# Optimization experiments

Measured on AMD Instinct MI355X. Metric: run time of the kernel, lower is better.

Reference implementation:

```python
import jax, jax.numpy as jnp
import numpy as np

N, D, K, V, H, F_ = 4096, 128, 64, 64, 4, 256
EPS = 1e-5


def _layer_norm(x, g, b):
    m = jnp.mean(x, axis=-1, keepdims=True)
    v = jnp.mean((x - m) ** 2, axis=-1, keepdims=True)
    return (x - m) * jax.lax.rsqrt(v + EPS) * g + b


def setup_inputs() -> dict:
    key = jax.random.key(0)
    ks = jax.random.split(key, 20)
    s_in = (2.0 / D) ** 0.5  # kaiming-ish scale for q/k/v projections
    inp = {
        "x": jax.random.normal(ks[0], (N, D), jnp.float32),
        "rpe": jax.random.normal(ks[1], (5, N, N), jnp.float32) * 0.02,
        "Wq": jax.random.normal(ks[2], (H, D, K), jnp.float32) * s_in,
        "bq": jnp.zeros((H, K), jnp.float32),
        "Wk": jax.random.normal(ks[3], (H, D, K), jnp.float32) * s_in,
        "bk": jnp.zeros((H, K), jnp.float32),
        "Wv": jax.random.normal(ks[4], (H, D, V), jnp.float32) * s_in,
        "bv": jnp.zeros((H, V), jnp.float32),
        "rpe_w": jax.random.normal(ks[5], (5,), jnp.float32) * (1.0 / 5.0) ** 0.5,
        "rpe_b": jnp.zeros((), jnp.float32),
        "Wo": jax.random.normal(ks[6], (H * V, D), jnp.float32) * (1.0 / (H * V)) ** 0.5,
        "bo": jnp.zeros((D,), jnp.float32),
        "W1": jax.random.normal(ks[7], (D, F_), jnp.float32) * (1.0 / D) ** 0.5,
        "b1": jnp.zeros((F_,), jnp.float32),
        "W2": jax.random.normal(ks[8], (F_, D), jnp.float32) * (1.0 / F_) ** 0.5,
        "b2": jnp.zeros((D,), jnp.float32),
        "ln1_g": jnp.ones((D,), jnp.float32),
        "ln1_b": jnp.zeros((D,), jnp.float32),
        "ln2_g": jnp.ones((D,), jnp.float32),
        "ln2_b": jnp.zeros((D,), jnp.float32),
    }
    return inp


def reference(x, rpe, Wq, bq, Wk, bk, Wv, bv, rpe_w, rpe_b, Wo, bo,
              W1, b1, W2, b2, ln1_g, ln1_b, ln2_g, ln2_b):
    # ReLU'd per-head projections (vectorized over heads): [H, N, K/V]
    q = jax.nn.relu(jnp.einsum("nd,hdk->hnk", x, Wq) + bq[:, None, :])
    k = jax.nn.relu(jnp.einsum("nd,hdk->hnk", x, Wk) + bk[:, None, :])
    v = jax.nn.relu(jnp.einsum("nd,hdv->hnv", x, Wv) + bv[:, None, :])
    scores = jnp.einsum("hnk,hmk->hnm", q, k) / jnp.sqrt(jnp.asarray(K, x.dtype))
    attn = jax.nn.softmax(scores, axis=-1)  # torch dim=1 on 2D == last axis
    o = jnp.einsum("hnm,hmv->hnv", attn, v)
    mho = jnp.transpose(o, (1, 0, 2)).reshape(N, H * V)  # concat heads
    # RPE: Linear(5->1) over channel axis -> [N, N], then left-matmul
    rpe_weights = jnp.einsum("fnm,f->nm", rpe, rpe_w) + rpe_b
    adjusted = rpe_weights @ mho
    proj = adjusted @ Wo + bo
    x1 = _layer_norm(x + proj, ln1_g, ln1_b)  # dropout is identity (eval)
    ffn = jax.nn.relu(x1 @ W1 + b1) @ W2 + b2
    return _layer_norm(x1 + ffn, ln2_g, ln2_b)
```

## Files before the change

kernel.cpp:

```cpp
#include <hip/hip_runtime.h>

typedef __attribute__((ext_vector_type(8))) short bf16x8;
typedef __attribute__((ext_vector_type(4))) float f32x4;

#define N_TOK 4096
#define NC_ATT 8
#define NC_GEMM 8

static __device__ __forceinline__ ushort f2bf(float f) {
    union { float f; unsigned u; } x; x.f = f;
    unsigned u = x.u;
    unsigned r = (u + 0x7FFFu + ((u >> 16) & 1u)) >> 16;
    return (ushort)r;
}
static __device__ __forceinline__ unsigned pkbf(float a, float b) {
    unsigned r;
    asm("v_cvt_pk_bf16_f32 %0, %1, %2" : "=v"(r) : "v"(a), "v"(b));
    return r;
}
static __device__ __forceinline__ float bf2f(ushort u) {
    union { unsigned u; float f; } x; x.u = (unsigned)u << 16; return x.f;
}

__global__ void prep_all(const float* __restrict__ x,
                         const float* __restrict__ Wq, const float* __restrict__ Wk,
                         const float* __restrict__ Wv, const float* __restrict__ Wo,
                         const float* __restrict__ W1, const float* __restrict__ W2,
                         ushort* __restrict__ xb, ushort* __restrict__ WqT,
                         ushort* __restrict__ WkT, ushort* __restrict__ WvT,
                         ushort* __restrict__ WoT, ushort* __restrict__ W1T,
                         ushort* __restrict__ W2T) {
    int i = blockIdx.x * 256 + threadIdx.x;
    if (i < 131072) {
        float4 v = ((const float4*)x)[i];
        ushort4 o;
        o.x = f2bf(v.x); o.y = f2bf(v.y); o.z = f2bf(v.z); o.w = f2bf(v.w);
        ((ushort4*)xb)[i] = o;
        return;
    }
    int j = i - 131072;
    int t = j >> 15, e = j & 32767;
    if (t < 3) {
        const float* src = (t == 0 ? Wq : t == 1 ? Wk : Wv);
        ushort* dst = (t == 0 ? WqT : t == 1 ? WkT : WvT);
        int h = e >> 13, rem = e & 8191, d = rem >> 6, k = rem & 63;
        dst[h * 8192 + k * 128 + d] = f2bf(src[e]);
    } else if (t == 3) {
        int r = e >> 7, c = e & 127;
        WoT[c * 256 + r] = f2bf(Wo[e]);
    } else if (t == 4) {
        int r = e >> 8, c = e & 255;
        W1T[c * 128 + r] = f2bf(W1[e]);
    } else {
        int r = e >> 7, c = e & 127;
        W2T[c * 256 + r] = f2bf(W2[e]);
    }
}

__global__ __launch_bounds__(256) void qkv_proj(
    const ushort* __restrict__ xb, const ushort* __restrict__ WqT,
    const ushort* __restrict__ WkT, const ushort* __restrict__ WvT,
    const float* __restrict__ bq, const float* __restrict__ bk, const float* __restrict__ bv,
    ushort* __restrict__ qb, ushort* __restrict__ kb, ushort* __restrict__ vT) {
    int m0 = blockIdx.x * 64;
    int h = blockIdx.y & 3, which = blockIdx.y >> 2;
    int wave = threadIdx.x >> 6, lane = threadIdx.x & 63;
    int fr = lane & 15, kg = lane >> 4;
    int wm = m0 + wave * 16;
    const ushort* WT = (which == 0 ? WqT : which == 1 ? WkT : WvT) + (long)h * 64 * 128;
    const float* bias = (which == 0 ? bq : which == 1 ? bk : bv) + h * 64;
    f32x4 acc[4] = {};
    for (int k0 = 0; k0 < 128; k0 += 32) {
        bf16x8 a = *(const bf16x8*)(xb + (long)(wm + fr) * 128 + k0 + kg * 8);
#pragma unroll
        for (int t = 0; t < 4; ++t) {
            bf16x8 b = *(const bf16x8*)(WT + (long)(t * 16 + fr) * 128 + k0 + kg * 8);
            acc[t] = __builtin_amdgcn_mfma_f32_16x16x32_bf16(a, b, acc[t], 0, 0, 0);
        }
    }
    int rb = wm + kg * 4;
#pragma unroll
    for (int t = 0; t < 4; ++t) {
        int col = t * 16 + fr;
        float bs = bias[col];
        if (which == 2) {
            ushort4 o;
            o.x = f2bf(fmaxf(acc[t][0] + bs, 0.f));
            o.y = f2bf(fmaxf(acc[t][1] + bs, 0.f));
            o.z = f2bf(fmaxf(acc[t][2] + bs, 0.f));
            o.w = f2bf(fmaxf(acc[t][3] + bs, 0.f));
            *(ushort4*)(vT + ((long)h * 64 + col) * N_TOK + rb) = o;
        } else {
            ushort* dst = (which == 0 ? qb : kb) + (long)h * N_TOK * 64;
            float scl = (which == 0) ? 0.125f * 1.44269504f : 1.0f;
#pragma unroll
            for (int r = 0; r < 4; ++r)
                dst[(long)(rb + r) * 64 + col] = f2bf(fmaxf(acc[t][r] + bs, 0.f) * scl);
        }
    }
}

__global__ __launch_bounds__(512, 6) void fused_rpe_attn(
    const float* __restrict__ rpe, const float* __restrict__ rpe_w,
    const float* __restrict__ rpe_b, ushort* __restrict__ rpeW,
    const ushort* __restrict__ qb, const ushort* __restrict__ kb,
    const ushort* __restrict__ vT, ushort* __restrict__ opart,
    float* __restrict__ mlpart) {
    __shared__ ushort Kt[2][64 * 64];
    __shared__ ushort Vt[2][64 * 64];
    __shared__ ushort Pl[8][16 * 64];
    int bid = blockIdx.x;
    int idx = bid >> 1;
    if ((bid & 1) == 0) {
        const long QUADS = (long)N_TOK * N_TOK / 4;
        float w0 = rpe_w[0], w1 = rpe_w[1], w2 = rpe_w[2], w3 = rpe_w[3], w4 = rpe_w[4];
        float bb = rpe_b[0];
        const float4* p = (const float4*)rpe;
        for (long i = (long)idx * 512 + threadIdx.x; i < QUADS; i += (long)1024 * 512) {
            float4 a0 = p[i];
            float4 a1 = p[i + QUADS];
            float4 a2 = p[i + 2 * QUADS];
            float4 a3 = p[i + 3 * QUADS];
            float4 a4 = p[i + 4 * QUADS];
            ushort4 o;
            unsigned lo = pkbf(bb + w0 * a0.x + w1 * a1.x + w2 * a2.x + w3 * a3.x + w4 * a4.x,
                               bb + w0 * a0.y + w1 * a1.y + w2 * a2.y + w3 * a3.y + w4 * a4.y);
            unsigned hi = pkbf(bb + w0 * a0.z + w1 * a1.z + w2 * a2.z + w3 * a3.z + w4 * a4.z,
                               bb + w0 * a0.w + w1 * a1.w + w2 * a2.w + w3 * a3.w + w4 * a4.w);
            o.x = (ushort)lo; o.y = (ushort)(lo >> 16);
            o.z = (ushort)hi; o.w = (ushort)(hi >> 16);
            ((ushort4*)rpeW)[i] = o;
        }
        return;
    }
    int qt = idx & 31, h = (idx >> 5) & 3, cz = idx >> 7;
    int w = threadIdx.x >> 6, lane = threadIdx.x & 63;
    int fr = lane & 15, kg = lane >> 4;
    int lr = lane >> 3, lc = lane & 7;
    int swz = (lc ^ (lr & 7)) * 8;
    const ushort* qh = qb + (long)h * N_TOK * 64;
    const ushort* kh = kb + (long)h * N_TOK * 64;
    const ushort* vh = vT + (long)h * 64 * N_TOK;
    int q0 = qt * 128 + w * 16;
    bf16x8 qf0 = *(const bf16x8*)(qh + (long)(q0 + fr) * 64 + kg * 8);
    bf16x8 qf1 = *(const bf16x8*)(qh + (long)(q0 + fr) * 64 + 32 + kg * 8);
    f32x4 o[4] = {};
    float lsum = 0.f;
    int nbase = cz * (N_TOK / NC_ATT);
    auto stage = [&](int buf, int s) {
        int n0 = nbase + s * 64;
        int row = w * 8 + lr;
        __builtin_amdgcn_global_load_lds(
            (const __attribute__((address_space(1))) unsigned int*)(kh + (long)(n0 + row) * 64 + swz),
            (__attribute__((address_space(3))) unsigned int*)(&Kt[buf][w * 512]), 16, 0, 0);
        __builtin_amdgcn_global_load_lds(
            (const __attribute__((address_space(1))) unsigned int*)(vh + (long)row * N_TOK + n0 + swz),
            (__attribute__((address_space(3))) unsigned int*)(&Vt[buf][w * 512]), 16, 0, 0);
    };
    stage(0, 0);
    __syncthreads();
    const int NS = (N_TOK / NC_ATT) / 64;
    for (int s = 0; s < NS; ++s) {
        int buf = s & 1;
        if (s + 1 < NS) stage(buf ^ 1, s + 1);
        f32x4 sc[4] = {};
        __builtin_amdgcn_s_setprio(1);
#pragma unroll
        for (int t = 0; t < 4; ++t) {
            int row = t * 16 + fr;
            bf16x8 k0 = *(const bf16x8*)(&Kt[buf][row * 64 + ((kg * 8) ^ ((row & 7) * 8))]);
            bf16x8 k1 = *(const bf16x8*)(&Kt[buf][row * 64 + ((32 + kg * 8) ^ ((row & 7) * 8))]);
            sc[t] = __builtin_amdgcn_mfma_f32_16x16x32_bf16(k0, qf0, sc[t], 0, 0, 0);
            sc[t] = __builtin_amdgcn_mfma_f32_16x16x32_bf16(k1, qf1, sc[t], 0, 0, 0);
        }
        __builtin_amdgcn_s_setprio(0);
#pragma unroll
        for (int t = 0; t < 4; ++t)
#pragma unroll
            for (int r = 0; r < 4; ++r) {
                float p = exp2f(sc[t][r]);
                sc[t][r] = p;
                lsum += p;
            }
#pragma unroll
        for (int t = 0; t < 4; ++t) {
            uint2 u;
            u.x = pkbf(sc[t][0], sc[t][1]);
            u.y = pkbf(sc[t][2], sc[t][3]);
            *(uint2*)(&Pl[w][fr * 64 + ((t * 16 + kg * 4) ^ ((fr & 7) * 8))]) = u;
        }
        __builtin_amdgcn_s_setprio(1);
#pragma unroll
        for (int ks = 0; ks < 2; ++ks) {
            bf16x8 pf = *(const bf16x8*)(&Pl[w][fr * 64 + ((ks * 32 + kg * 8) ^ ((fr & 7) * 8))]);
#pragma unroll
            for (int t = 0; t < 4; ++t) {
                int row = t * 16 + fr;
                bf16x8 b = *(const bf16x8*)(&Vt[buf][row * 64 + ((ks * 32 + kg * 8) ^ ((row & 7) * 8))]);
                o[t] = __builtin_amdgcn_mfma_f32_16x16x32_bf16(pf, b, o[t], 0, 0, 0);
            }
        }
        __builtin_amdgcn_s_setprio(0);
        __syncthreads();
    }
    lsum += __shfl_xor(lsum, 16);
    lsum += __shfl_xor(lsum, 32);
    float linv = 1.0f / lsum;
    float lq[4];
#pragma unroll
    for (int r = 0; r < 4; ++r) lq[r] = __shfl(linv, kg * 4 + r);
    ushort* ob = opart + (((long)cz * 4 + h) * N_TOK + q0 + kg * 4) * 64;
#pragma unroll
    for (int t = 0; t < 4; ++t)
#pragma unroll
        for (int r = 0; r < 4; ++r)
            ob[(long)r * 64 + t * 16 + fr] = f2bf(o[t][r] * lq[r]);
    if (lane < 16)
        mlpart[((long)cz * 4 + h) * N_TOK + q0 + lane] = lsum;
}

__global__ __launch_bounds__(256) void combine_wo(
    const ushort* __restrict__ opart, const float* __restrict__ mlpart,
    const ushort* __restrict__ WoT, ushort* __restrict__ PT) {
    int q0 = blockIdx.x * 16;
    int tid = threadIdx.x;
    __shared__ ushort mt[16 * 256];
    {
        int q = tid >> 4, cg = tid & 15;
        int h = cg >> 2;
        long qg = q0 + q;
        float L = 0.f, co[NC_ATT];
#pragma unroll
        for (int c = 0; c < NC_ATT; ++c) {
            co[c] = mlpart[((long)c * 4 + h) * N_TOK + qg];
            L += co[c];
        }
        float inv = 1.0f / L;
#pragma unroll
        for (int c = 0; c < NC_ATT; ++c) co[c] *= inv;
        float a[16];
#pragma unroll
        for (int j = 0; j < 16; ++j) a[j] = 0.f;
#pragma unroll
        for (int c = 0; c < NC_ATT; ++c) {
            const ushort* pr = opart + (((long)c * 4 + h) * N_TOK + qg) * 64 + (cg & 3) * 16;
            bf16x8 v0 = *(const bf16x8*)(pr);
            bf16x8 v1 = *(const bf16x8*)(pr + 8);
#pragma unroll
            for (int j = 0; j < 8; ++j) {
                a[j] += co[c] * bf2f((ushort)v0[j]);
                a[8 + j] += co[c] * bf2f((ushort)v1[j]);
            }
        }
        int c0 = cg * 16;
#pragma unroll
        for (int g = 0; g < 4; ++g) {
            uint2 u;
            u.x = pkbf(a[g * 4 + 0], a[g * 4 + 1]);
            u.y = pkbf(a[g * 4 + 2], a[g * 4 + 3]);
            *(uint2*)(&mt[q * 256 + ((c0 + g * 4) ^ ((q & 7) * 8))]) = u;
        }
    }
    __syncthreads();
    {
        int w = tid >> 6, lane = tid & 63;
        int fr = lane & 15, kg = lane >> 4;
        f32x4 acc[2] = {};
        for (int k0 = 0; k0 < 256; k0 += 32) {
            bf16x8 a0 = *(const bf16x8*)(WoT + (long)(w * 32 + fr) * 256 + k0 + kg * 8);
            bf16x8 a1 = *(const bf16x8*)(WoT + (long)(w * 32 + 16 + fr) * 256 + k0 + kg * 8);
            bf16x8 b = *(const bf16x8*)(&mt[fr * 256 + ((k0 + kg * 8) ^ ((fr & 7) * 8))]);
            acc[0] = __builtin_amdgcn_mfma_f32_16x16x32_bf16(a0, b, acc[0], 0, 0, 0);
            acc[1] = __builtin_amdgcn_mfma_f32_16x16x32_bf16(a1, b, acc[1], 0, 0, 0);
        }
#pragma unroll
        for (int dt = 0; dt < 2; ++dt)
#pragma unroll
            for (int r = 0; r < 4; ++r)
                PT[(long)(w * 32 + dt * 16 + kg * 4 + r) * N_TOK + q0 + fr] =
                    f2bf(acc[dt][r]);
    }
}

__global__ __launch_bounds__(512) void gemm_big2(
    const ushort* __restrict__ A, const ushort* __restrict__ PT,
    float* __restrict__ part) {
    int mt = blockIdx.x, cz = blockIdx.y;
    int tid = threadIdx.x;
    int w = tid >> 6, lane = tid & 63;
    int fr = lane & 15, kg = lane >> 4;
    int lr = lane >> 3, lc = lane & 7;
    int swz = (lc ^ (lr & 7)) * 8;
    int ms = w >> 1, nh = w & 1;
    __shared__ ushort At[2][64 * 64];
    __shared__ ushort Bt[2][128 * 64];
    int m0 = mt * 64;
    long kbase = (long)cz * (N_TOK / NC_GEMM);
    int arow = ms * 16 + fr;
    auto stage = [&](int buf, int s) {
        long kc = kbase + s * 64 + swz;
        int rowA = w * 8 + lr;
        __builtin_amdgcn_global_load_lds(
            (const __attribute__((address_space(1))) unsigned int*)(A + (long)(m0 + rowA) * N_TOK + kc),
            (__attribute__((address_space(3))) unsigned int*)(&At[buf][w * 512]), 16, 0, 0);
#pragma unroll
        for (int j = 0; j < 2; ++j) {
            int row = w * 16 + j * 8 + lr;
            __builtin_amdgcn_global_load_lds(
                (const __attribute__((address_space(1))) unsigned int*)(PT + (long)row * N_TOK + kc),
                (__attribute__((address_space(3))) unsigned int*)(&Bt[buf][(w * 2 + j) * 512]), 16, 0, 0);
        }
    };
    f32x4 acc[4] = {};
    stage(0, 0);
    __syncthreads();
    const int NS = (N_TOK / NC_GEMM) / 64;
    for (int s = 0; s < NS; ++s) {
        int buf = s & 1;
        if (s + 1 < NS) stage(buf ^ 1, s + 1);
        __builtin_amdgcn_s_setprio(1);
#pragma unroll
        for (int ks = 0; ks < 2; ++ks) {
            int c = ks * 32 + kg * 8;
            bf16x8 av = *(const bf16x8*)(&At[buf][arow * 64 + (c ^ ((arow & 7) * 8))]);
#pragma unroll
            for (int nf = 0; nf < 4; ++nf) {
                int row = nh * 64 + nf * 16 + fr;
                bf16x8 b = *(const bf16x8*)(&Bt[buf][row * 64 + (c ^ ((row & 7) * 8))]);
                acc[nf] = __builtin_amdgcn_mfma_f32_16x16x32_bf16(av, b, acc[nf], 0, 0, 0);
            }
        }
        __builtin_amdgcn_s_setprio(0);
        __syncthreads();
    }
    float* pb = part + ((long)cz * N_TOK + m0 + ms * 16 + kg * 4) * 128 + nh * 64 + fr;
#pragma unroll
    for (int nf = 0; nf < 4; ++nf)
#pragma unroll
        for (int r = 0; r < 4; ++r)
            pb[(long)r * 128 + nf * 16] = acc[nf][r];
}

__global__ __launch_bounds__(256) void megatail(
    const float* __restrict__ gpart, const float* __restrict__ bo,
    const float* __restrict__ x, const float* __restrict__ g1,
    const float* __restrict__ lb1, const ushort* __restrict__ W1T,
    const float* __restrict__ b1, const ushort* __restrict__ W2T,
    const float* __restrict__ b2, const float* __restrict__ g2,
    const float* __restrict__ lb2, float* __restrict__ out) {
    int r0 = blockIdx.x * 16;
    int tid = threadIdx.x;
    int w = tid >> 6, lane = tid & 63;
    int fr = lane & 15, kg = lane >> 4;
    __shared__ float x1f[16][132];
    __shared__ ushort x1b[16][128];
    __shared__ ushort hbuf[16][256];
    __shared__ float otile[16][132];
    int row = tid >> 4, c0 = (tid & 15) * 8;
    {
        float v[8];
        float4 s0 = {0.f, 0.f, 0.f, 0.f}, s1 = {0.f, 0.f, 0.f, 0.f};
#pragma unroll
        for (int c = 0; c < NC_GEMM; ++c) {
            const float* pr = gpart + ((long)c * N_TOK + r0 + row) * 128 + c0;
            float4 a = *(const float4*)(pr);
            float4 b = *(const float4*)(pr + 4);
            s0.x += a.x; s0.y += a.y; s0.z += a.z; s0.w += a.w;
            s1.x += b.x; s1.y += b.y; s1.z += b.z; s1.w += b.w;
        }
        const float* xr = x + (long)(r0 + row) * 128 + c0;
        v[0] = s0.x + bo[c0 + 0] + xr[0];
        v[1] = s0.y + bo[c0 + 1] + xr[1];
        v[2] = s0.z + bo[c0 + 2] + xr[2];
        v[3] = s0.w + bo[c0 + 3] + xr[3];
        v[4] = s1.x + bo[c0 + 4] + xr[4];
        v[5] = s1.y + bo[c0 + 5] + xr[5];
        v[6] = s1.z + bo[c0 + 6] + xr[6];
        v[7] = s1.w + bo[c0 + 7] + xr[7];
        float s = 0.f;
#pragma unroll
        for (int jj = 0; jj < 8; ++jj) s += v[jj];
#pragma unroll
        for (int off = 1; off < 16; off <<= 1) s += __shfl_xor(s, off);
        float mean = s * (1.0f / 128.0f);
        float ss = 0.f;
#pragma unroll
        for (int jj = 0; jj < 8; ++jj) { float d = v[jj] - mean; ss += d * d; }
#pragma unroll
        for (int off = 1; off < 16; off <<= 1) ss += __shfl_xor(ss, off);
        float rstd = rsqrtf(ss * (1.0f / 128.0f) + 1e-5f);
        union { bf16x8 vec; ushort us[8]; } pk8;
#pragma unroll
        for (int jj = 0; jj < 8; ++jj) {
            float y = (v[jj] - mean) * rstd * g1[c0 + jj] + lb1[c0 + jj];
            x1f[row][c0 + jj] = y;
            pk8.us[jj] = f2bf(y);
        }
        *(bf16x8*)(&x1b[row][c0 ^ ((row & 7) * 8)]) = pk8.vec;
    }
    __syncthreads();
    {
        f32x4 a1[4] = {};
#pragma unroll
        for (int ks = 0; ks < 4; ++ks) {
            bf16x8 a = *(const bf16x8*)(&x1b[fr][(ks * 32 + kg * 8) ^ ((fr & 7) * 8)]);
#pragma unroll
            for (int t = 0; t < 4; ++t) {
                bf16x8 b = *(const bf16x8*)(W1T + (long)(w * 64 + t * 16 + fr) * 128 + ks * 32 + kg * 8);
                a1[t] = __builtin_amdgcn_mfma_f32_16x16x32_bf16(a, b, a1[t], 0, 0, 0);
            }
        }
#pragma unroll
        for (int t = 0; t < 4; ++t) {
            int col = w * 64 + t * 16 + fr;
            float bs = b1[col];
#pragma unroll
            for (int r = 0; r < 4; ++r) {
                int rr = kg * 4 + r;
                hbuf[rr][col ^ ((rr & 7) * 8)] = f2bf(fmaxf(a1[t][r] + bs, 0.f));
            }
        }
    }
    __syncthreads();
    {
        f32x4 a2[2] = {};
#pragma unroll
        for (int ks = 0; ks < 8; ++ks) {
            bf16x8 a = *(const bf16x8*)(&hbuf[fr][(ks * 32 + kg * 8) ^ ((fr & 7) * 8)]);
#pragma unroll
            for (int t = 0; t < 2; ++t) {
                bf16x8 b = *(const bf16x8*)(W2T + (long)(w * 32 + t * 16 + fr) * 256 + ks * 32 + kg * 8);
                a2[t] = __builtin_amdgcn_mfma_f32_16x16x32_bf16(a, b, a2[t], 0, 0, 0);
            }
        }
#pragma unroll
        for (int t = 0; t < 2; ++t) {
            int col = w * 32 + t * 16 + fr;
            float bs = b2[col];
#pragma unroll
            for (int r = 0; r < 4; ++r) {
                int rr = kg * 4 + r;
                otile[rr][col] = a2[t][r] + bs + x1f[rr][col];
            }
        }
    }
    __syncthreads();
    {
        float v[8];
        float s = 0.f;
#pragma unroll
        for (int jj = 0; jj < 8; ++jj) { v[jj] = otile[row][c0 + jj]; s += v[jj]; }
#pragma unroll
        for (int off = 1; off < 16; off <<= 1) s += __shfl_xor(s, off);
        float mean = s * (1.0f / 128.0f);
        float ss = 0.f;
#pragma unroll
        for (int jj = 0; jj < 8; ++jj) { float d = v[jj] - mean; ss += d * d; }
#pragma unroll
        for (int off = 1; off < 16; off <<= 1) ss += __shfl_xor(ss, off);
        float rstd = rsqrtf(ss * (1.0f / 128.0f) + 1e-5f);
#pragma unroll
        for (int jj = 0; jj < 8; ++jj) {
            float y = (v[jj] - mean) * rstd * g2[c0 + jj] + lb2[c0 + jj];
            out[(long)(r0 + row) * 128 + c0 + jj] = y;
        }
    }
}

extern "C" void kernel_launch(void* const* d_in, const int* in_sizes, int n_in,
                              void* d_out, int out_size, void* d_ws, size_t ws_size,
                              hipStream_t stream) {
    const float* x     = (const float*)d_in[0];
    const float* rpe   = (const float*)d_in[1];
    const float* Wq    = (const float*)d_in[2];
    const float* bq    = (const float*)d_in[3];
    const float* Wk    = (const float*)d_in[4];
    const float* bk    = (const float*)d_in[5];
    const float* Wv    = (const float*)d_in[6];
    const float* bv    = (const float*)d_in[7];
    const float* rpe_w = (const float*)d_in[8];
    const float* rpe_b = (const float*)d_in[9];
    const float* Wo    = (const float*)d_in[10];
    const float* bo    = (const float*)d_in[11];
    const float* W1    = (const float*)d_in[12];
    const float* b1    = (const float*)d_in[13];
    const float* W2    = (const float*)d_in[14];
    const float* b2    = (const float*)d_in[15];
    const float* g1    = (const float*)d_in[16];
    const float* lb1   = (const float*)d_in[17];
    const float* g2    = (const float*)d_in[18];
    const float* lb2   = (const float*)d_in[19];

    char* wp = (char*)d_ws;
    auto alloc = [&](size_t sz) { char* p = wp; wp += (sz + 255) & ~(size_t)255; return p; };
    ushort* xb    = (ushort*)alloc((size_t)4096 * 128 * 2);
    ushort* WqT   = (ushort*)alloc((size_t)4 * 64 * 128 * 2);
    ushort* WkT   = (ushort*)alloc((size_t)4 * 64 * 128 * 2);
    ushort* WvT   = (ushort*)alloc((size_t)4 * 64 * 128 * 2);
    ushort* WoT   = (ushort*)alloc((size_t)128 * 256 * 2);
    ushort* W1T   = (ushort*)alloc((size_t)256 * 128 * 2);
    ushort* W2T   = (ushort*)alloc((size_t)128 * 256 * 2);
    ushort* qb    = (ushort*)alloc((size_t)4 * 4096 * 64 * 2);
    ushort* kbuf  = (ushort*)alloc((size_t)4 * 4096 * 64 * 2);
    ushort* vT    = (ushort*)alloc((size_t)4 * 64 * 4096 * 2);
    ushort* rpeW  = (ushort*)alloc((size_t)4096 * 4096 * 2);
    ushort* PTb   = (ushort*)alloc((size_t)128 * 4096 * 2);
    ushort* opart = (ushort*)alloc((size_t)NC_ATT * 4 * 4096 * 64 * 2);
    float*  mlprt = (float*)alloc((size_t)NC_ATT * 4 * 4096 * 4);
    float*  gpart = (float*)alloc((size_t)NC_GEMM * 4096 * 128 * 4);

    prep_all<<<1280, 256, 0, stream>>>(x, Wq, Wk, Wv, Wo, W1, W2,
                                       xb, WqT, WkT, WvT, WoT, W1T, W2T);
    qkv_proj<<<dim3(64, 12), 256, 0, stream>>>(xb, WqT, WkT, WvT, bq, bk, bv, qb, kbuf, vT);
    fused_rpe_attn<<<2048, 512, 0, stream>>>(rpe, rpe_w, rpe_b, rpeW,
                                             qb, kbuf, vT, opart, mlprt);
    combine_wo<<<256, 256, 0, stream>>>(opart, mlprt, WoT, PTb);
    gemm_big2<<<dim3(64, NC_GEMM), 512, 0, stream>>>(rpeW, PTb, gpart);
    megatail<<<256, 256, 0, stream>>>(gpart, bo, x, g1, lb1, W1T, b1, W2T, b2,
                                      g2, lb2, (float*)d_out);
}
```

Baseline: 135.3 us.

## Split RPE weighted-sum stream across qkv, attention and combine kernels

The bandwidth-heavy RPE channel reduction (5x N^2 floats into bf16) was previously hidden only behind the attention kernel. It is now split into three ranges (about 15%, 65% and 20%), each handled by extra blocks appended to the qkv projection, attention and combine_wo launches. The aim is to overlap more of the memory streaming with the smaller compute kernels so the attention kernel is no longer bound by the RPE traffic. The cost is larger grids and possible contention that could slow the qkv and combine kernels.

```diff
diff --git a/kernel.cpp b/kernel.cpp
--- a/kernel.cpp
+++ b/kernel.cpp
@@ -6,6 +6,10 @@
 #define N_TOK 4096
 #define NC_ATT 8
 #define NC_GEMM 8
+
+#define RPE_QUADS 4194304L
+#define RPE_Q1 629145L
+#define RPE_Q2 3355443L
 
 static __device__ __forceinline__ ushort f2bf(float f) {
     union { float f; unsigned u; } x; x.f = f;
@@ -20,6 +24,30 @@
 }
 static __device__ __forceinline__ float bf2f(ushort u) {
     union { unsigned u; float f; } x; x.u = (unsigned)u << 16; return x.f;
+}
+
+static __device__ __forceinline__ void rpe_stream_role(
+    const float* __restrict__ rpe, const float* __restrict__ rpe_w,
+    const float* __restrict__ rpe_b, ushort* __restrict__ rpeW,
+    long lo, long hi, int rb, long stride) {
+    float w0 = rpe_w[0], w1 = rpe_w[1], w2 = rpe_w[2], w3 = rpe_w[3], w4 = rpe_w[4];
+    float bb = rpe_b[0];
+    const float4* p = (const float4*)rpe;
+    for (long i = lo + (long)rb * blockDim.x + threadIdx.x; i < hi; i += stride) {
+        float4 a0 = p[i];
+        float4 a1 = p[i + RPE_QUADS];
+        float4 a2 = p[i + 2 * RPE_QUADS];
+        float4 a3 = p[i + 3 * RPE_QUADS];
+        float4 a4 = p[i + 4 * RPE_QUADS];
+        ushort4 o;
+        unsigned lov = pkbf(bb + w0 * a0.x + w1 * a1.x + w2 * a2.x + w3 * a3.x + w4 * a4.x,
+                            bb + w0 * a0.y + w1 * a1.y + w2 * a2.y + w3 * a3.y + w4 * a4.y);
+        unsigned hiv = pkbf(bb + w0 * a0.z + w1 * a1.z + w2 * a2.z + w3 * a3.z + w4 * a4.z,
+                            bb + w0 * a0.w + w1 * a1.w + w2 * a2.w + w3 * a3.w + w4 * a4.w);
+        o.x = (ushort)lov; o.y = (ushort)(lov >> 16);
+        o.z = (ushort)hiv; o.w = (ushort)(hiv >> 16);
+        ((ushort4*)rpeW)[i] = o;
+    }
 }
 
 __global__ void prep_all(const float* __restrict__ x,
@@ -57,13 +85,21 @@
     }
 }
 
-__global__ __launch_bounds__(256) void qkv_proj(
+__global__ __launch_bounds__(256) void fused_rpe_qkv(
+    const float* __restrict__ rpe, const float* __restrict__ rpe_w,
+    const float* __restrict__ rpe_b, ushort* __restrict__ rpeW,
     const ushort* __restrict__ xb, const ushort* __restrict__ WqT,
     const ushort* __restrict__ WkT, const ushort* __restrict__ WvT,
     const float* __restrict__ bq, const float* __restrict__ bk, const float* __restrict__ bv,
     ushort* __restrict__ qb, ushort* __restrict__ kb, ushort* __restrict__ vT) {
-    int m0 = blockIdx.x * 64;
-    int h = blockIdx.y & 3, which = blockIdx.y >> 2;
+    int bid = blockIdx.x;
+    if (bid >= 768) {
+        rpe_stream_role(rpe, rpe_w, rpe_b, rpeW, 0L, RPE_Q1, bid - 768, (long)1024 * 256);
+        return;
+    }
+    int m0 = (bid & 63) * 64;
+    int y = bid >> 6;
+    int h = y & 3, which = y >> 2;
     int wave = threadIdx.x >> 6, lane = threadIdx.x & 63;
     int fr = lane & 15, kg = lane >> 4;
     int wm = m0 + wave * 16;
@@ -112,25 +148,7 @@
     int bid = blockIdx.x;
     int idx = bid >> 1;
     if ((bid & 1) == 0) {
-        const long QUADS = (long)N_TOK * N_TOK / 4;
-        float w0 = rpe_w[0], w1 = rpe_w[1], w2 = rpe_w[2], w3 = rpe_w[3], w4 = rpe_w[4];
-        float bb = rpe_b[0];
-        const float4* p = (const float4*)rpe;
-        for (long i = (long)idx * 512 + threadIdx.x; i < QUADS; i += (long)1024 * 512) {
-            float4 a0 = p[i];
-            float4 a1 = p[i + QUADS];
-            float4 a2 = p[i + 2 * QUADS];
-            float4 a3 = p[i + 3 * QUADS];
-            float4 a4 = p[i + 4 * QUADS];
-            ushort4 o;
-            unsigned lo = pkbf(bb + w0 * a0.x + w1 * a1.x + w2 * a2.x + w3 * a3.x + w4 * a4.x,
-                               bb + w0 * a0.y + w1 * a1.y + w2 * a2.y + w3 * a3.y + w4 * a4.y);
-            unsigned hi = pkbf(bb + w0 * a0.z + w1 * a1.z + w2 * a2.z + w3 * a3.z + w4 * a4.z,
-                               bb + w0 * a0.w + w1 * a1.w + w2 * a2.w + w3 * a3.w + w4 * a4.w);
-            o.x = (ushort)lo; o.y = (ushort)(lo >> 16);
-            o.z = (ushort)hi; o.w = (ushort)(hi >> 16);
-            ((ushort4*)rpeW)[i] = o;
-        }
+        rpe_stream_role(rpe, rpe_w, rpe_b, rpeW, RPE_Q1, RPE_Q2, idx, (long)1024 * 512);
         return;
     }
     int qt = idx & 31, h = (idx >> 5) & 3, cz = idx >> 7;
@@ -219,10 +237,17 @@
         mlpart[((long)cz * 4 + h) * N_TOK + q0 + lane] = lsum;
 }
 
-__global__ __launch_bounds__(256) void combine_wo(
+__global__ __launch_bounds__(256) void fused_rpe_cw(
+    const float* __restrict__ rpe, const float* __restrict__ rpe_w,
+    const float* __restrict__ rpe_b, ushort* __restrict__ rpeW,
     const ushort* __restrict__ opart, const float* __restrict__ mlpart,
     const ushort* __restrict__ WoT, ushort* __restrict__ PT) {
-    int q0 = blockIdx.x * 16;
+    int bid = blockIdx.x;
+    if (bid >= 256) {
+        rpe_stream_role(rpe, rpe_w, rpe_b, rpeW, RPE_Q2, RPE_QUADS, bid - 256, (long)768 * 256);
+        return;
+    }
+    int q0 = bid * 16;
     int tid = threadIdx.x;
     __shared__ ushort mt[16 * 256];
     {
@@ -511,10 +536,12 @@
 
     prep_all<<<1280, 256, 0, stream>>>(x, Wq, Wk, Wv, Wo, W1, W2,
                                        xb, WqT, WkT, WvT, WoT, W1T, W2T);
-    qkv_proj<<<dim3(64, 12), 256, 0, stream>>>(xb, WqT, WkT, WvT, bq, bk, bv, qb, kbuf, vT);
+    fused_rpe_qkv<<<1792, 256, 0, stream>>>(rpe, rpe_w, rpe_b, rpeW,
+                                            xb, WqT, WkT, WvT, bq, bk, bv, qb, kbuf, vT);
     fused_rpe_attn<<<2048, 512, 0, stream>>>(rpe, rpe_w, rpe_b, rpeW,
                                              qb, kbuf, vT, opart, mlprt);
-    combine_wo<<<256, 256, 0, stream>>>(opart, mlprt, WoT, PTb);
+    fused_rpe_cw<<<1024, 256, 0, stream>>>(rpe, rpe_w, rpe_b, rpeW,
+                                           opart, mlprt, WoT, PTb);
     gemm_big2<<<dim3(64, NC_GEMM), 512, 0, stream>>>(rpeW, PTb, gpart);
     megatail<<<256, 256, 0, stream>>>(gpart, bo, x, g1, lb1, W1T, b1, W2T, b2,
                                       g2, lb2, (float*)d_out);
```

Result: faster. 131.3 us, median of 2 (-2.9%).
